# Optimization experiments

Measured on AMD Instinct MI355X. Metric: run time of the kernel, lower is better.

Reference implementation:

```python
import jax, jax.numpy as jnp
import numpy as np
import math

T, B, D, H, L, C = 2048, 64, 256, 256, 2, 2
HIGHWAY_BIAS = 0.0
# SRU rescale factor for the highway skip term (rescale=True)
SCALE_X = (1.0 + math.exp(HIGHWAY_BIAS * 2)) ** 0.5


def setup_inputs() -> dict:
    key = jax.random.key(0)
    ks = jax.random.split(key, 8)
    s = 1.0 / np.sqrt(D)
    x = jax.random.normal(ks[0], (T, B, D), dtype=jnp.float32)
    # per-layer SRU weights: W [D, 3H] -> (x_tilde, f, r); bias [2H] -> (b_f, b_r)
    W1 = jax.random.uniform(ks[1], (D, 3 * H), jnp.float32, -s, s)
    b1 = jnp.zeros((2 * H,), jnp.float32)
    W2 = jax.random.uniform(ks[2], (H, 3 * H), jnp.float32, -s, s)
    b2 = jnp.zeros((2 * H,), jnp.float32)
    lin_W = jax.random.uniform(ks[3], (H, C), jnp.float32, -s, s)
    lin_b = jnp.zeros((C,), jnp.float32)
    return {"x": x, "W1": W1, "b1": b1, "W2": W2, "b2": b2,
            "lin_W": lin_W, "lin_b": lin_b}


def _sru_layer(x, W, b):
    # x: [T, B, D]; W: [D, 3H]; b: [2H]. Skip term uses raw x (D == H).
    U = jnp.einsum('tbd,dk->tbk', x, W)           # [T, B, 3H]
    x_tilde, f_raw, r_raw = jnp.split(U, 3, axis=-1)
    b_f, b_r = jnp.split(b, 2)
    f = jax.nn.sigmoid(f_raw + b_f + HIGHWAY_BIAS)  # [T, B, H]
    r = jax.nn.sigmoid(r_raw + b_r)                 # [T, B, H]

    def step(c, inp):
        f_t, xt_t = inp
        c = f_t * c + (1.0 - f_t) * xt_t
        return c, c

    c0 = jnp.zeros(x.shape[1:], x.dtype)            # [B, H]
    _, cs = jax.lax.scan(step, c0, (f, x_tilde))    # cs: [T, B, H]
    h = r * cs + (1.0 - r) * (x * SCALE_X)          # highway skip (rescaled)
    return h


def reference(x, W1, b1, W2, b2, lin_W, lin_b):
    h1 = _sru_layer(x, W1, b1)
    h2 = _sru_layer(h1, W2, b2)
    last = h2[-1]                                   # [B, H] (last timestep)
    # Dropout in eval mode = identity (deterministic reference)
    return last @ lin_W + lin_b                     # [B, C]
```

## Files before the change

kernel.cpp:

```cpp
#include <hip/hip_runtime.h>
#include <hip/hip_bf16.h>
#include <stdint.h>

#define T_LEN 2048
#define B_SZ  64
#define H_SZ  256
#define NH3   768
#define M_SZ  (T_LEN * B_SZ)
#define NC    64
#define TC    32
#define SCALE_X_F 1.41421356237309515f

typedef __attribute__((ext_vector_type(8))) short short8;
typedef __attribute__((ext_vector_type(4))) float f32x4;

__device__ __forceinline__ float sigmoidf_(float z) {
    return 1.0f / (1.0f + __expf(-z));
}
__device__ __forceinline__ unsigned short f2bf(float f) {
    unsigned u = __float_as_uint(f);
    return (unsigned short)((u + 0x7FFFu + ((u >> 16) & 1u)) >> 16);
}
__device__ __forceinline__ float bf2f(unsigned short s) {
    return __uint_as_float(((unsigned)s) << 16);
}

__global__ void k_convert_x(const float* __restrict__ x, unsigned short* __restrict__ xb) {
    int i = blockIdx.x * blockDim.x + threadIdx.x;
    const float4* in = (const float4*)x;
    float4 a = in[i * 2];
    float4 b = in[i * 2 + 1];
    short8 o;
    o[0] = (short)f2bf(a.x); o[1] = (short)f2bf(a.y);
    o[2] = (short)f2bf(a.z); o[3] = (short)f2bf(a.w);
    o[4] = (short)f2bf(b.x); o[5] = (short)f2bf(b.y);
    o[6] = (short)f2bf(b.z); o[7] = (short)f2bf(b.w);
    *(short8*)&xb[(size_t)i * 8] = o;
}

__global__ void k_prep_w(const float* __restrict__ W, unsigned short* __restrict__ Wt) {
    int i = blockIdx.x * 256 + threadIdx.x;
    int n = i >> 8, k = i & 255;
    Wt[i] = f2bf(W[(size_t)k * NH3 + n]);
}

__global__ void k_gemm(const unsigned short* __restrict__ A,
                       const unsigned short* __restrict__ Bt,
                       unsigned short* __restrict__ C) {
    __shared__ alignas(16) unsigned short As[128 * 64];
    __shared__ alignas(16) unsigned short Bs[128 * 64];

    int bid = blockIdx.x;
    int mt = bid / 6, nt = bid % 6;
    int mbase = mt * 128, nbase = nt * 128;
    int tid = threadIdx.x;
    int w = tid >> 6, l = tid & 63;
    int r16 = l & 15, kg = l >> 4;
    int wr = w >> 1, wc = w & 1;

    f32x4 acc[4][4];
    #pragma unroll
    for (int m = 0; m < 4; ++m)
        #pragma unroll
        for (int n = 0; n < 4; ++n) {
            f32x4 z = {0.f, 0.f, 0.f, 0.f};
            acc[m][n] = z;
        }

    for (int kt = 0; kt < 4; ++kt) {
        int k0 = kt * 64;
        #pragma unroll
        for (int p = 0; p < 4; ++p) {
            int row = w * 32 + p * 8 + (l >> 3);
            int col = (l & 7) * 8;
            const unsigned short* ga = A  + (size_t)(mbase + row) * 256 + k0 + col;
            const unsigned short* gb = Bt + (size_t)(nbase + row) * 256 + k0 + col;
            __builtin_amdgcn_global_load_lds(
                (const __attribute__((address_space(1))) void*)ga,
                (__attribute__((address_space(3))) void*)&As[(w * 4 + p) * 512], 16, 0, 0);
            __builtin_amdgcn_global_load_lds(
                (const __attribute__((address_space(1))) void*)gb,
                (__attribute__((address_space(3))) void*)&Bs[(w * 4 + p) * 512], 16, 0, 0);
        }
        __syncthreads();

        short8 af[4][2], bfv[4][2];
        #pragma unroll
        for (int m = 0; m < 4; ++m)
            #pragma unroll
            for (int kk = 0; kk < 2; ++kk)
                af[m][kk] = *(const short8*)&As[(wr * 64 + m * 16 + r16) * 64 + kk * 32 + kg * 8];
        #pragma unroll
        for (int n = 0; n < 4; ++n)
            #pragma unroll
            for (int kk = 0; kk < 2; ++kk)
                bfv[n][kk] = *(const short8*)&Bs[(wc * 64 + n * 16 + r16) * 64 + kk * 32 + kg * 8];

        #pragma unroll
        for (int m = 0; m < 4; ++m)
            #pragma unroll
            for (int n = 0; n < 4; ++n)
                #pragma unroll
                for (int kk = 0; kk < 2; ++kk)
                    acc[m][n] = __builtin_amdgcn_mfma_f32_16x16x32_bf16(
                        af[m][kk], bfv[n][kk], acc[m][n], 0, 0, 0);
        __syncthreads();
    }

    #pragma unroll
    for (int m = 0; m < 4; ++m)
        #pragma unroll
        for (int n = 0; n < 4; ++n) {
            int row0 = mbase + wr * 64 + m * 16 + kg * 4;
            int col  = nbase + wc * 64 + n * 16 + r16;
            #pragma unroll
            for (int r = 0; r < 4; ++r)
                C[(size_t)(row0 + r) * NH3 + col] = f2bf(acc[m][n][r]);
        }
}

__global__ void k_passA(const unsigned short* __restrict__ U, const float* __restrict__ bias,
                        float* __restrict__ P, float* __restrict__ S) {
    int ci = blockIdx.x >> 6;
    int b  = blockIdx.x & 63;
    int h  = threadIdx.x;
    float bfv = bias[h];
    size_t base = ((size_t)(ci * TC) * B_SZ + b) * NH3 + h;
    float c = 0.f, pr = 1.f;
    #pragma unroll 4
    for (int t = 0; t < TC; ++t) {
        float xt = bf2f(U[base]);
        float fr = bf2f(U[base + 256]);
        float f = sigmoidf_(fr + bfv);
        c = f * c + (1.f - f) * xt;
        pr *= f;
        base += (size_t)B_SZ * NH3;
    }
    int o = blockIdx.x * 256 + h;
    P[o] = pr;
    S[o] = c;
}

__global__ void k_passB(const float* __restrict__ P, const float* __restrict__ S,
                        float* __restrict__ cin) {
    int b = blockIdx.x, h = threadIdx.x;
    int idx = b * 256 + h;
    float c = 0.f;
    #pragma unroll 8
    for (int ci = 0; ci < NC; ++ci) {
        cin[ci * 16384 + idx] = c;
        c = P[ci * 16384 + idx] * c + S[ci * 16384 + idx];
    }
    cin[NC * 16384 + idx] = c;
}

__global__ void k_passC(const unsigned short* __restrict__ U, const float* __restrict__ bias,
                        const unsigned short* __restrict__ xb, const float* __restrict__ cin,
                        unsigned short* __restrict__ hout) {
    int ci = blockIdx.x >> 6, b = blockIdx.x & 63, h = threadIdx.x;
    float bfv = bias[h], brv = bias[256 + h];
    float c = cin[blockIdx.x * 256 + h];
    size_t base  = ((size_t)(ci * TC) * B_SZ + b) * NH3 + h;
    size_t xbase = ((size_t)(ci * TC) * B_SZ + b) * H_SZ + h;
    #pragma unroll 4
    for (int t = 0; t < TC; ++t) {
        float xt = bf2f(U[base]);
        float fr = bf2f(U[base + 256]);
        float rr = bf2f(U[base + 512]);
        float f = sigmoidf_(fr + bfv);
        float r = sigmoidf_(rr + brv);
        c = f * c + (1.f - f) * xt;
        float xv = bf2f(xb[xbase]);
        hout[xbase] = f2bf(r * c + (1.f - r) * xv * SCALE_X_F);
        base  += (size_t)B_SZ * NH3;
        xbase += (size_t)B_SZ * H_SZ;
    }
}

__global__ void k_final(const unsigned short* __restrict__ U, const float* __restrict__ bias,
                        const unsigned short* __restrict__ h1, const float* __restrict__ cin,
                        const float* __restrict__ lw, const float* __restrict__ lb,
                        float* __restrict__ out) {
    int b = blockIdx.x, h = threadIdx.x;
    float c = cin[NC * 16384 + b * 256 + h];
    size_t ub = ((size_t)(T_LEN - 1) * B_SZ + b) * NH3;
    float r = sigmoidf_(bf2f(U[ub + 512 + h]) + bias[256 + h]);
    float xl = bf2f(h1[((size_t)(T_LEN - 1) * B_SZ + b) * H_SZ + h]);
    float hv = r * c + (1.f - r) * xl * SCALE_X_F;
    float p0 = hv * lw[h * 2];
    float p1 = hv * lw[h * 2 + 1];
    #pragma unroll
    for (int off = 32; off; off >>= 1) {
        p0 += __shfl_down(p0, off);
        p1 += __shfl_down(p1, off);
    }
    __shared__ float s0[4], s1[4];
    int wid = h >> 6, lane = h & 63;
    if (lane == 0) { s0[wid] = p0; s1[wid] = p1; }
    __syncthreads();
    if (h == 0) {
        out[b * 2]     = s0[0] + s0[1] + s0[2] + s0[3] + lb[0];
        out[b * 2 + 1] = s1[0] + s1[1] + s1[2] + s1[3] + lb[1];
    }
}

extern "C" void kernel_launch(void* const* d_in, const int* in_sizes, int n_in,
                              void* d_out, int out_size, void* d_ws, size_t ws_size,
                              hipStream_t stream) {
    const float* x   = (const float*)d_in[0];
    const float* W1  = (const float*)d_in[1];
    const float* b1  = (const float*)d_in[2];
    const float* W2  = (const float*)d_in[3];
    const float* b2  = (const float*)d_in[4];
    const float* lw  = (const float*)d_in[5];
    const float* lb  = (const float*)d_in[6];
    float* out = (float*)d_out;

    char* ws = (char*)d_ws;
    unsigned short* U   = (unsigned short*)ws;
    unsigned short* xb  = (unsigned short*)(ws + 201326592);
    unsigned short* h1  = (unsigned short*)(ws + 268435456);
    unsigned short* Wt1 = (unsigned short*)(ws + 335544320);
    unsigned short* Wt2 = (unsigned short*)(ws + 335937536);
    float* Pbuf = (float*)(ws + 336330752);
    float* Sbuf = (float*)(ws + 340525056);
    float* cin  = (float*)(ws + 344719360);

    k_convert_x<<<16384, 256, 0, stream>>>(x, xb);
    k_prep_w<<<768, 256, 0, stream>>>(W1, Wt1);
    k_prep_w<<<768, 256, 0, stream>>>(W2, Wt2);

    k_gemm<<<6144, 256, 0, stream>>>(xb, Wt1, U);
    k_passA<<<4096, 256, 0, stream>>>(U, b1, Pbuf, Sbuf);
    k_passB<<<64, 256, 0, stream>>>(Pbuf, Sbuf, cin);
    k_passC<<<4096, 256, 0, stream>>>(U, b1, xb, cin, h1);

    k_gemm<<<6144, 256, 0, stream>>>(h1, Wt2, U);
    k_passA<<<4096, 256, 0, stream>>>(U, b2, Pbuf, Sbuf);
    k_passB<<<64, 256, 0, stream>>>(Pbuf, Sbuf, cin);
    k_final<<<64, 256, 0, stream>>>(U, b2, h1, cin, lw, lb, out);
}
```

Measured before the change: 386.4 us.

## Skip layer-2 r-gate GEMM, swizzle LDS, stage GEMM output through shared memory

The layer-2 GEMM now computes only the x_tilde and f columns (512 instead of 768). The r gate is needed only at the last timestep, so k_final computes it directly from h1's last row and W2, which removes a third of the second GEMM's compute and writes. The GEMM gains an XOR-swizzled LDS layout to avoid bank conflicts, an XCD-aware block remap, and a coalesced 16-byte epilogue that goes through shared memory. It adds an extra LDS round trip and a barrier in the epilogue, and k_final now does a small per-batch matvec.

```diff
diff --git a/kernel.cpp b/kernel.cpp
--- a/kernel.cpp
+++ b/kernel.cpp
@@ -44,19 +44,26 @@
     Wt[i] = f2bf(W[(size_t)k * NH3 + n]);
 }
 
+template <int NT, int CS>
 __global__ void k_gemm(const unsigned short* __restrict__ A,
                        const unsigned short* __restrict__ Bt,
                        unsigned short* __restrict__ C) {
-    __shared__ alignas(16) unsigned short As[128 * 64];
-    __shared__ alignas(16) unsigned short Bs[128 * 64];
-
-    int bid = blockIdx.x;
-    int mt = bid / 6, nt = bid % 6;
+    __shared__ alignas(16) unsigned short smem[128 * 128];
+    unsigned short* As = smem;
+    unsigned short* Bs = smem + 8192;
+
+    const int cpx = (1024 * NT) / 8;
+    int orig = blockIdx.x;
+    int wgid = (orig & 7) * cpx + (orig >> 3);
+    int mt = wgid / NT, nt = wgid % NT;
     int mbase = mt * 128, nbase = nt * 128;
+
     int tid = threadIdx.x;
     int w = tid >> 6, l = tid & 63;
     int r16 = l & 15, kg = l >> 4;
     int wr = w >> 1, wc = w & 1;
+    int scol = ((l & 7) ^ (l >> 3)) * 8;
+    int srow = (l >> 3);
 
     f32x4 acc[4][4];
     #pragma unroll
@@ -71,10 +78,9 @@
         int k0 = kt * 64;
         #pragma unroll
         for (int p = 0; p < 4; ++p) {
-            int row = w * 32 + p * 8 + (l >> 3);
-            int col = (l & 7) * 8;
-            const unsigned short* ga = A  + (size_t)(mbase + row) * 256 + k0 + col;
-            const unsigned short* gb = Bt + (size_t)(nbase + row) * 256 + k0 + col;
+            int row = w * 32 + p * 8 + srow;
+            const unsigned short* ga = A  + (size_t)(mbase + row) * 256 + k0 + scol;
+            const unsigned short* gb = Bt + (size_t)(nbase + row) * 256 + k0 + scol;
             __builtin_amdgcn_global_load_lds(
                 (const __attribute__((address_space(1))) void*)ga,
                 (__attribute__((address_space(3))) void*)&As[(w * 4 + p) * 512], 16, 0, 0);
@@ -86,15 +92,21 @@
 
         short8 af[4][2], bfv[4][2];
         #pragma unroll
-        for (int m = 0; m < 4; ++m)
+        for (int m = 0; m < 4; ++m) {
+            int arow = wr * 64 + m * 16 + r16;
+            int sw = (arow & 7) << 3;
             #pragma unroll
             for (int kk = 0; kk < 2; ++kk)
-                af[m][kk] = *(const short8*)&As[(wr * 64 + m * 16 + r16) * 64 + kk * 32 + kg * 8];
-        #pragma unroll
-        for (int n = 0; n < 4; ++n)
+                af[m][kk] = *(const short8*)&As[arow * 64 + ((kk * 32 + kg * 8) ^ sw)];
+        }
+        #pragma unroll
+        for (int n = 0; n < 4; ++n) {
+            int brow = wc * 64 + n * 16 + r16;
+            int sw = (brow & 7) << 3;
             #pragma unroll
             for (int kk = 0; kk < 2; ++kk)
-                bfv[n][kk] = *(const short8*)&Bs[(wc * 64 + n * 16 + r16) * 64 + kk * 32 + kg * 8];
+                bfv[n][kk] = *(const short8*)&Bs[brow * 64 + ((kk * 32 + kg * 8) ^ sw)];
+        }
 
         #pragma unroll
         for (int m = 0; m < 4; ++m)
@@ -111,21 +123,30 @@
     for (int m = 0; m < 4; ++m)
         #pragma unroll
         for (int n = 0; n < 4; ++n) {
-            int row0 = mbase + wr * 64 + m * 16 + kg * 4;
-            int col  = nbase + wc * 64 + n * 16 + r16;
-            #pragma unroll
-            for (int r = 0; r < 4; ++r)
-                C[(size_t)(row0 + r) * NH3 + col] = f2bf(acc[m][n][r]);
-        }
+            int col = wc * 64 + n * 16 + r16;
+            #pragma unroll
+            for (int r = 0; r < 4; ++r) {
+                int row = wr * 64 + m * 16 + kg * 4 + r;
+                smem[row * 128 + (col ^ ((row & 7) << 3))] = f2bf(acc[m][n][r]);
+            }
+        }
+    __syncthreads();
+    #pragma unroll
+    for (int i = 0; i < 8; ++i) {
+        int slot = i * 256 + tid;
+        int row = slot >> 4, seg = slot & 15;
+        short8 v = *(const short8*)&smem[row * 128 + ((seg * 8) ^ ((row & 7) << 3))];
+        *(short8*)&C[(size_t)(mbase + row) * CS + nbase + seg * 8] = v;
+    }
 }
 
 __global__ void k_passA(const unsigned short* __restrict__ U, const float* __restrict__ bias,
-                        float* __restrict__ P, float* __restrict__ S) {
+                        float* __restrict__ P, float* __restrict__ S, int stride) {
     int ci = blockIdx.x >> 6;
     int b  = blockIdx.x & 63;
     int h  = threadIdx.x;
     float bfv = bias[h];
-    size_t base = ((size_t)(ci * TC) * B_SZ + b) * NH3 + h;
+    size_t base = ((size_t)(ci * TC) * B_SZ + b) * stride + h;
     float c = 0.f, pr = 1.f;
     #pragma unroll 4
     for (int t = 0; t < TC; ++t) {
@@ -134,7 +155,7 @@
         float f = sigmoidf_(fr + bfv);
         c = f * c + (1.f - f) * xt;
         pr *= f;
-        base += (size_t)B_SZ * NH3;
+        base += (size_t)B_SZ * stride;
     }
     int o = blockIdx.x * 256 + h;
     P[o] = pr;
@@ -177,16 +198,22 @@
     }
 }
 
-__global__ void k_final(const unsigned short* __restrict__ U, const float* __restrict__ bias,
-                        const unsigned short* __restrict__ h1, const float* __restrict__ cin,
+__global__ void k_final(const unsigned short* __restrict__ h1, const float* __restrict__ cin,
+                        const float* __restrict__ W2, const float* __restrict__ b2,
                         const float* __restrict__ lw, const float* __restrict__ lb,
                         float* __restrict__ out) {
     int b = blockIdx.x, h = threadIdx.x;
+    __shared__ float hrow[256];
+    size_t hb = ((size_t)(T_LEN - 1) * B_SZ + b) * H_SZ;
+    hrow[h] = bf2f(h1[hb + h]);
+    __syncthreads();
+    float rr = 0.f;
+    #pragma unroll 8
+    for (int k = 0; k < 256; ++k)
+        rr += hrow[k] * W2[(size_t)k * NH3 + 512 + h];
+    float r = sigmoidf_(rr + b2[256 + h]);
     float c = cin[NC * 16384 + b * 256 + h];
-    size_t ub = ((size_t)(T_LEN - 1) * B_SZ + b) * NH3;
-    float r = sigmoidf_(bf2f(U[ub + 512 + h]) + bias[256 + h]);
-    float xl = bf2f(h1[((size_t)(T_LEN - 1) * B_SZ + b) * H_SZ + h]);
-    float hv = r * c + (1.f - r) * xl * SCALE_X_F;
+    float hv = r * c + (1.f - r) * hrow[h] * SCALE_X_F;
     float p0 = hv * lw[h * 2];
     float p1 = hv * lw[h * 2 + 1];
     #pragma unroll
@@ -228,15 +255,15 @@
 
     k_convert_x<<<16384, 256, 0, stream>>>(x, xb);
     k_prep_w<<<768, 256, 0, stream>>>(W1, Wt1);
-    k_prep_w<<<768, 256, 0, stream>>>(W2, Wt2);
-
-    k_gemm<<<6144, 256, 0, stream>>>(xb, Wt1, U);
-    k_passA<<<4096, 256, 0, stream>>>(U, b1, Pbuf, Sbuf);
+    k_prep_w<<<512, 256, 0, stream>>>(W2, Wt2);
+
+    k_gemm<6, NH3><<<6144, 256, 0, stream>>>(xb, Wt1, U);
+    k_passA<<<4096, 256, 0, stream>>>(U, b1, Pbuf, Sbuf, NH3);
     k_passB<<<64, 256, 0, stream>>>(Pbuf, Sbuf, cin);
     k_passC<<<4096, 256, 0, stream>>>(U, b1, xb, cin, h1);
 
-    k_gemm<<<6144, 256, 0, stream>>>(h1, Wt2, U);
-    k_passA<<<4096, 256, 0, stream>>>(U, b2, Pbuf, Sbuf);
+    k_gemm<4, 512><<<4096, 256, 0, stream>>>(h1, Wt2, U);
+    k_passA<<<4096, 256, 0, stream>>>(U, b2, Pbuf, Sbuf, 512);
     k_passB<<<64, 256, 0, stream>>>(Pbuf, Sbuf, cin);
-    k_final<<<64, 256, 0, stream>>>(U, b2, h1, cin, lw, lb, out);
-}
+    k_final<<<64, 256, 0, stream>>>(h1, cin, W2, b2, lw, lb, out);
+}
```

Result: slower. 413.6 us (+7.0%).
